# Performance work log

Hardware: AMD Instinct MI355X
Metric: run time of the kernel (lower is better)

Reference implementation:

```python
import jax, jax.numpy as jnp
import numpy as np

H, D = 16, 64  # num_heads, head_dim (hidden=1024)


def _rel_shift(x):
    # Transformer-XL skewing: x [B,H,T,L] -> shifted [B,H,T,T]
    B, Hh, T, L = x.shape
    x = jnp.pad(x, ((0, 0), (0, 0), (0, 0), (1, 0)))
    x = x.reshape(B, Hh, L + 1, T)[:, :, 1:, :]
    return x.reshape(B, Hh, T, L)[:, :, :, :T]


def setup_inputs() -> dict:
    key = jax.random.key(0)
    ks = jax.random.split(key, 9)
    B, T, hid = 2, 2048, 1024
    s = 0.02
    return {
        "x": jax.random.normal(ks[0], (B, T, hid), jnp.float32),
        "pos_emb": jax.random.normal(ks[1], (T, hid), jnp.float32),
        "Wq": jax.random.normal(ks[2], (hid, hid), jnp.float32) * s,
        "Wk": jax.random.normal(ks[3], (hid, hid), jnp.float32) * s,
        "Wv": jax.random.normal(ks[4], (hid, hid), jnp.float32) * s,
        "Wo": jax.random.normal(ks[5], (hid, hid), jnp.float32) * s,
        "Wrel": jax.random.normal(ks[6], (hid, hid), jnp.float32) * s,
        "bias_u": jax.random.normal(ks[7], (H, D), jnp.float32) * s,
        "bias_v": jax.random.normal(ks[8], (H, D), jnp.float32) * s,
    }


def reference(x, pos_emb, Wq, Wk, Wv, Wo, Wrel, bias_u, bias_v):
    B, T, hid = x.shape
    scale = D ** (-0.5)
    # projections (torch Linear: y = x @ W.T), reshape to [B,H,T,D]
    q = (x @ Wq.T).reshape(B, T, H, D).transpose(0, 2, 1, 3)
    k = (x @ Wk.T).reshape(B, T, H, D).transpose(0, 2, 1, 3)
    v = (x @ Wv.T).reshape(B, T, H, D).transpose(0, 2, 1, 3)
    # content score with bias_u
    content = jnp.einsum('bhtd,bhsd->bhts', q + bias_u[None, :, None, :], k)
    # positional score with bias_v against projected relative keys [H,L,D]
    rel_k = (pos_emb @ Wrel.T).reshape(-1, H, D).transpose(1, 0, 2)
    pos_score = jnp.einsum('bhtd,hld->bhtl', q + bias_v[None, :, None, :], rel_k)
    pos_score = _rel_shift(pos_score)
    scores = (content + pos_score) * scale
    attn = jax.nn.softmax(scores, axis=-1)
    out = jnp.einsum('bhts,bhsd->bhtd', attn, v)
    out = out.transpose(0, 2, 1, 3).reshape(B, T, hid)
    return out @ Wo.T
```

## Files before the change

kernel.cpp:

```cpp
#include <hip/hip_runtime.h>
#include <hip/hip_bf16.h>

#define T_SEQ 2048
#define HID   1024
#define NH    16
#define HD    64
#define NB    2

typedef __bf16 bf16_t;
typedef bf16_t bf16x8 __attribute__((ext_vector_type(8)));
typedef bf16_t bf16x4 __attribute__((ext_vector_type(4)));
typedef float  f32x4  __attribute__((ext_vector_type(4)));

static __device__ __forceinline__ f32x4 mfma16(bf16x8 a, bf16x8 b, f32x4 c) {
    return __builtin_amdgcn_mfma_f32_16x16x32_bf16(a, b, c, 0, 0, 0);
}

static __device__ __forceinline__ void gll16(const bf16_t* g, bf16_t* l) {
    __builtin_amdgcn_global_load_lds(
        (const __attribute__((address_space(1))) void*)g,
        (__attribute__((address_space(3))) void*)l, 16, 0, 0);
}

__global__ __launch_bounds__(256) void cvt_all(
    const float* __restrict__ x, const float* __restrict__ pos,
    const float* __restrict__ wq, const float* __restrict__ wk,
    const float* __restrict__ wv, const float* __restrict__ wo,
    const float* __restrict__ wrel,
    bf16_t* __restrict__ xb, bf16_t* __restrict__ pb,
    bf16_t* __restrict__ wqb, bf16_t* __restrict__ wkb,
    bf16_t* __restrict__ wvb, bf16_t* __restrict__ wob,
    bf16_t* __restrict__ wrelb)
{
    int blk = blockIdx.x;
    const float* in; bf16_t* out;
    if (blk < 2048)      { in = x;   out = xb; }
    else if (blk < 3072) { in = pos; out = pb; blk -= 2048; }
    else {
        const int wi = (blk - 3072) >> 9; blk = (blk - 3072) & 511;
        switch (wi) {
            case 0:  in = wq;   out = wqb;   break;
            case 1:  in = wk;   out = wkb;   break;
            case 2:  in = wv;   out = wvb;   break;
            case 3:  in = wo;   out = wob;   break;
            default: in = wrel; out = wrelb; break;
        }
    }
    const int i = blk * 256 + threadIdx.x;
    const float4* p = (const float4*)(in + (size_t)i * 8);
    float4 a0 = p[0], a1 = p[1];
    bf16x8 v;
    v[0]=(bf16_t)a0.x; v[1]=(bf16_t)a0.y; v[2]=(bf16_t)a0.z; v[3]=(bf16_t)a0.w;
    v[4]=(bf16_t)a1.x; v[5]=(bf16_t)a1.y; v[6]=(bf16_t)a1.z; v[7]=(bf16_t)a1.w;
    *(bf16x8*)(out + (size_t)i * 8) = v;
}

template<int OMODE>
__global__ __launch_bounds__(256) void gemm_bb(const bf16_t* __restrict__ A,
                                               const bf16_t* __restrict__ W,
                                               void* __restrict__ outv, int M, int cpx) {
    const int hw = blockIdx.x;
    const int logical = (hw & 7) * cpx + (hw >> 3);
    const int mt = logical >> 3, nt = logical & 7;
    const int row0 = mt * 128, col0 = nt * 128;
    const int tid = threadIdx.x;
    const int w = tid >> 6, lane = tid & 63;
    const int wr = (w >> 1) * 64, wc = (w & 1) * 64;
    const int lr = lane & 15, lkg = lane >> 4;
    const int kd = lkg * 8;

    __shared__ bf16_t Al[128*64];
    __shared__ bf16_t Bl[128*64];

    const int rsh   = lane >> 3;
    const int colSw = ((lane & 7) * 8) ^ (rsh << 3);
    const int rBase = 8*w + rsh;

    f32x4 acc[4][4] = {};

    for (int t = 0; t < 16; ++t) {
        const int k0 = t * 64;
        if (t) __syncthreads();
#pragma unroll
        for (int i = 0; i < 4; ++i) {
            const int r = rBase + 32*i;
            gll16(A + (size_t)(row0 + r)*HID + k0 + colSw, &Al[i*2048 + w*512]);
            gll16(W + (size_t)(col0 + r)*HID + k0 + colSw, &Bl[i*2048 + w*512]);
        }
        __syncthreads();
#pragma unroll
        for (int ks = 0; ks < 2; ++ks) {
            bf16x8 af[4], bq[4];
#pragma unroll
            for (int i = 0; i < 4; ++i) {
                const int ar = wr + i*16 + lr;
                af[i] = *(const bf16x8*)&Al[ar*64 + ((ks*32 + kd) ^ ((ar & 7) << 3))];
                const int br = wc + i*16 + lr;
                bq[i] = *(const bf16x8*)&Bl[br*64 + ((ks*32 + kd) ^ ((br & 7) << 3))];
            }
#pragma unroll
            for (int i = 0; i < 4; ++i)
#pragma unroll
                for (int j = 0; j < 4; ++j)
                    acc[i][j] = mfma16(af[i], bq[j], acc[i][j]);
        }
    }

    const int rb = lkg * 4;
#pragma unroll
    for (int i = 0; i < 4; ++i) {
#pragma unroll
        for (int j = 0; j < 4; ++j) {
            const int col = col0 + wc + j*16 + lr;
            const int row = row0 + wr + i*16 + rb;
            if (OMODE == 0) {
                bf16_t* ob = (bf16_t*)outv;
#pragma unroll
                for (int r = 0; r < 4; ++r)
                    ob[(size_t)(row + r) * HID + col] = (bf16_t)acc[i][j][r];
            } else if (OMODE == 1) {
                const int bb = row >> 11, tt = row & (T_SEQ - 1);
                const int hh = col >> 6,  d = col & 63;
                bf16x4 pk;
#pragma unroll
                for (int r = 0; r < 4; ++r) pk[r] = (bf16_t)acc[i][j][r];
                *(bf16x4*)((bf16_t*)outv + ((size_t)((bb*NH + hh)*HD + d))*T_SEQ + tt) = pk;
            } else {
                float* of = (float*)outv;
#pragma unroll
                for (int r = 0; r < 4; ++r)
                    of[(size_t)(row + r) * HID + col] = acc[i][j][r];
            }
        }
    }
}

template<int NSPLIT>
__global__ __launch_bounds__(256) void attn_kernel(
    const bf16_t* __restrict__ Q, const bf16_t* __restrict__ K,
    const bf16_t* __restrict__ VT, const bf16_t* __restrict__ RK,
    const float* __restrict__ bias_u, const float* __restrict__ bias_v,
    bf16_t* __restrict__ AO, float* __restrict__ PO, float* __restrict__ ML,
    int cpx)
{
    const int hw = blockIdx.x;
    const int logical = (hw & 7) * cpx + (hw >> 3);
    const int tile = logical & 31;
    int h, b, split;
    if (NSPLIT == 1) {
        split = 0; h = (logical >> 5) & 15; b = logical >> 9;
    } else {
        split = (logical >> 5) & 1; h = (logical >> 6) & 15; b = logical >> 10;
    }

    const int w = threadIdx.x >> 6, lane = threadIdx.x & 63;
    const int t0 = tile * 64;
    const int lr = lane & 15, lkg = lane >> 4;
    const int kd = lkg * 8;

    __shared__ bf16_t Kl[64*64];
    __shared__ bf16_t Vl[64*64];
    __shared__ bf16_t R1l[128*64];
    __shared__ bf16_t R2l[128*64];
    __shared__ float  pp[4][16][84];
    __shared__ bf16_t pl[4][16][72];

    const int tb = t0 + w * 16;

    bf16x8 aqu[2], aqv[2], aqv2[2];
    {
        const int t  = tb + lr;
        const int t2 = (t + 1 < T_SEQ) ? t + 1 : T_SEQ - 1;
        const bf16_t* qp  = Q + ((size_t)(b*T_SEQ + t )*NH + h)*HD;
        const bf16_t* qp2 = Q + ((size_t)(b*T_SEQ + t2)*NH + h)*HD;
        const float* bu = bias_u + h*HD;
        const float* bv = bias_v + h*HD;
#pragma unroll
        for (int f = 0; f < 2; ++f) {
            const int k0 = f*32 + kd;
            bf16x8 q1 = *(const bf16x8*)(qp  + k0);
            bf16x8 q2 = *(const bf16x8*)(qp2 + k0);
#pragma unroll
            for (int j = 0; j < 8; ++j) {
                const float fu = bu[k0+j], fv = bv[k0+j];
                aqu [f][j] = (bf16_t)(((float)q1[j] + fu) * 0.125f);
                aqv [f][j] = (bf16_t)(((float)q1[j] + fv) * 0.125f);
                aqv2[f][j] = (bf16_t)(((float)q2[j] + fv) * 0.125f);
            }
        }
    }

    float m_run = -1e30f, l_run = 0.0f;
    f32x4 oacc[4];
    f32x4 zf = {0.f, 0.f, 0.f, 0.f};
#pragma unroll
    for (int nf = 0; nf < 4; ++nf) oacc[nf] = zf;

    const bf16_t* Kb = K  + (size_t)(b*T_SEQ)*HID + h*HD;
    const bf16_t* Vb = VT + (size_t)((b*NH + h)*HD)*T_SEQ;
    const bf16_t* Rb = RK + h*HD;
    const int d15 = 15 - lr;
    const int sBeg = split * (T_SEQ / NSPLIT);

    const int rsh   = lane >> 3;
    const int colSw = ((lane & 7) * 8) ^ (rsh << 3);
    const int kvRow = 16*w + rsh;
    const int rRow  = 32*w + rsh;

    for (int ss = 0; ss < T_SEQ / NSPLIT; ss += 64) {
        const int s0 = sBeg + ss;
        const int r1base = s0 - t0 + T_SEQ - 64;
        const int r2base = s0 - t0 - 65;
        const bool anyB1 = (s0 <= t0 + 63);
        const bool anyB2 = (s0 >= t0 - 61);

        __syncthreads();
#pragma unroll
        for (int i = 0; i < 2; ++i) {
            const int r = kvRow + 8*i;
            gll16(Kb + (size_t)(s0 + r)*HID + colSw, &Kl[(2*w + i)*512]);
            gll16(Vb + (size_t)r*T_SEQ + s0 + colSw, &Vl[(2*w + i)*512]);
        }
        if (anyB1) {
#pragma unroll
            for (int i = 0; i < 4; ++i) {
                const long g = (long)(r1base + rRow + 8*i);
                gll16(Rb + g*HID + colSw, &R1l[(4*w + i)*512]);
            }
        }
        if (anyB2) {
#pragma unroll
            for (int i = 0; i < 4; ++i) {
                const long g = (long)(r2base + rRow + 8*i);
                gll16(Rb + g*HID + colSw, &R2l[(4*w + i)*512]);
            }
        }
        __syncthreads();

        f32x4 sc[4];
#pragma unroll
        for (int j = 0; j < 4; ++j) {
            const int row = j*16 + lr;
            const int sw = (row & 7) << 3;
            bf16x8 a0 = *(const bf16x8*)&Kl[row*64 + (kd ^ sw)];
            bf16x8 a1 = *(const bf16x8*)&Kl[row*64 + ((32 + kd) ^ sw)];
            sc[j] = mfma16(a1, aqu[1], mfma16(a0, aqu[0], zf));
        }

        if (s0 <= tb + 15) {
#pragma unroll
            for (int jf = 0; jf < 5; ++jf) {
                const int rr = 48 - 16*w + jf*16 + lr;
                const int sw = (rr & 7) << 3;
                bf16x8 a0 = *(const bf16x8*)&R1l[rr*64 + (kd ^ sw)];
                bf16x8 a1 = *(const bf16x8*)&R1l[rr*64 + ((32 + kd) ^ sw)];
                f32x4 c = mfma16(a1, aqv[1], mfma16(a0, aqv[0], zf));
                *(f32x4*)&pp[w][lr][jf*16 + 4*lkg] = c;
            }
            if (s0 <= tb - 63) {
#pragma unroll
                for (int j = 0; j < 4; ++j)
#pragma unroll
                    for (int r = 0; r < 4; ++r)
                        sc[j][r] += pp[w][lr][16*j + 4*lkg + r + d15];
            } else {
#pragma unroll
                for (int j = 0; j < 4; ++j)
#pragma unroll
                    for (int r = 0; r < 4; ++r) {
                        const int sof = 16*j + 4*lkg + r;
                        const int dt  = (s0 + sof) - (tb + lr);
                        const float v = pp[w][lr][sof + d15];
                        sc[j][r] += (dt <= 0) ? v : 0.0f;
                    }
            }
        }
        if (s0 >= tb - 61) {
#pragma unroll
            for (int jf = 0; jf < 5; ++jf) {
                const int rr = 48 - 16*w + jf*16 + lr;
                const int sw = (rr & 7) << 3;
                bf16x8 a0 = *(const bf16x8*)&R2l[rr*64 + (kd ^ sw)];
                bf16x8 a1 = *(const bf16x8*)&R2l[rr*64 + ((32 + kd) ^ sw)];
                f32x4 c = mfma16(a1, aqv2[1], mfma16(a0, aqv2[0], zf));
                *(f32x4*)&pp[w][lr][jf*16 + 4*lkg] = c;
            }
            if (s0 >= tb + 17) {
#pragma unroll
                for (int j = 0; j < 4; ++j)
#pragma unroll
                    for (int r = 0; r < 4; ++r)
                        sc[j][r] += pp[w][lr][16*j + 4*lkg + r + d15];
            } else {
#pragma unroll
                for (int j = 0; j < 4; ++j)
#pragma unroll
                    for (int r = 0; r < 4; ++r) {
                        const int sof = 16*j + 4*lkg + r;
                        const int dt  = (s0 + sof) - (tb + lr);
                        const float v = pp[w][lr][sof + d15];
                        sc[j][r] += (dt >= 2) ? v : 0.0f;
                    }
            }
        }

        float mx = fmaxf(fmaxf(fmaxf(sc[0][0], sc[0][1]), fmaxf(sc[0][2], sc[0][3])),
                         fmaxf(fmaxf(sc[1][0], sc[1][1]), fmaxf(sc[1][2], sc[1][3])));
        mx = fmaxf(mx, fmaxf(fmaxf(fmaxf(sc[2][0], sc[2][1]), fmaxf(sc[2][2], sc[2][3])),
                             fmaxf(fmaxf(sc[3][0], sc[3][1]), fmaxf(sc[3][2], sc[3][3]))));
        mx = fmaxf(mx, __shfl_xor(mx, 16, 64));
        mx = fmaxf(mx, __shfl_xor(mx, 32, 64));
        const float mnew = fmaxf(m_run, mx);
        const float fac = __expf(m_run - mnew);
        float sum = 0.0f;
#pragma unroll
        for (int j = 0; j < 4; ++j) {
            bf16x4 pk;
#pragma unroll
            for (int r = 0; r < 4; ++r) {
                const float p = __expf(sc[j][r] - mnew);
                sum += p;
                pk[r] = (bf16_t)p;
            }
            *(bf16x4*)&pl[w][lr][16*j + 4*lkg] = pk;
        }
        sum += __shfl_xor(sum, 16, 64);
        sum += __shfl_xor(sum, 32, 64);
        l_run = l_run * fac + sum;
        m_run = mnew;

#pragma unroll
        for (int r = 0; r < 4; ++r) {
            const float facq = __shfl(fac, 4*lkg + r, 64);
#pragma unroll
            for (int nf = 0; nf < 4; ++nf) oacc[nf][r] *= facq;
        }

        bf16x8 pa0 = *(const bf16x8*)(&pl[w][lr][kd]);
        bf16x8 pa1 = *(const bf16x8*)(&pl[w][lr][32 + kd]);
#pragma unroll
        for (int nf = 0; nf < 4; ++nf) {
            const int row = nf*16 + lr;
            const int sw = (row & 7) << 3;
            bf16x8 b0 = *(const bf16x8*)&Vl[row*64 + (kd ^ sw)];
            bf16x8 b1 = *(const bf16x8*)&Vl[row*64 + ((32 + kd) ^ sw)];
            oacc[nf] = mfma16(pa1, b1, mfma16(pa0, b0, oacc[nf]));
        }
    }

    if (NSPLIT == 1) {
        const float linv = 1.0f / l_run;
#pragma unroll
        for (int r = 0; r < 4; ++r) {
            const float lq = __shfl(linv, 4*lkg + r, 64);
            const int t = tb + 4*lkg + r;
#pragma unroll
            for (int nf = 0; nf < 4; ++nf)
                AO[(size_t)(b*T_SEQ + t)*HID + h*HD + nf*16 + lr] = (bf16_t)(oacc[nf][r] * lq);
        }
    } else {
        float* po = PO + (((size_t)split*NB*NH + b*NH + h)*T_SEQ)*HD;
#pragma unroll
        for (int r = 0; r < 4; ++r)
#pragma unroll
            for (int nf = 0; nf < 4; ++nf)
                po[(size_t)(tb + 4*lkg + r)*HD + nf*16 + lr] = oacc[nf][r];
        if (lkg == 0) {
            float* ml = ML + ((size_t)split*NB*NH + b*NH + h)*2*T_SEQ;
            ml[tb + lr] = m_run;
            ml[T_SEQ + tb + lr] = l_run;
        }
    }
}

__global__ __launch_bounds__(256) void combine_kernel(
    const float* __restrict__ PO, const float* __restrict__ ML,
    bf16_t* __restrict__ AO)
{
    const int idx = blockIdx.x * 256 + threadIdx.x;
    const int t = idx & (T_SEQ - 1);
    const int h = (idx >> 11) & (NH - 1);
    const int b = idx >> 15;
    const size_t poS = (size_t)NB*NH*T_SEQ*HD;
    const size_t mlS = (size_t)NB*NH*2*T_SEQ;
    const float* po1 = PO + (((size_t)b*NH + h)*T_SEQ + t)*HD;
    const float* po2 = po1 + poS;
    const float* ml1 = ML + ((size_t)b*NH + h)*2*T_SEQ;
    const float* ml2 = ml1 + mlS;
    const float m1 = ml1[t], l1 = ml1[T_SEQ + t];
    const float m2 = ml2[t], l2 = ml2[T_SEQ + t];
    const float M  = fmaxf(m1, m2);
    float f1 = __expf(m1 - M), f2 = __expf(m2 - M);
    const float linv = 1.0f / (f1*l1 + f2*l2);
    f1 *= linv; f2 *= linv;
    bf16_t* ao = AO + ((size_t)b*T_SEQ + t)*HID + h*HD;
#pragma unroll
    for (int d = 0; d < HD; d += 8) {
        f32x4 a0 = *(const f32x4*)(po1 + d), a1 = *(const f32x4*)(po1 + d + 4);
        f32x4 c0 = *(const f32x4*)(po2 + d), c1 = *(const f32x4*)(po2 + d + 4);
        bf16x8 o;
#pragma unroll
        for (int j = 0; j < 4; ++j) {
            o[j]     = (bf16_t)(f1*a0[j] + f2*c0[j]);
            o[4 + j] = (bf16_t)(f1*a1[j] + f2*c1[j]);
        }
        *(bf16x8*)(ao + d) = o;
    }
}

extern "C" void kernel_launch(void* const* d_in, const int* in_sizes, int n_in,
                              void* d_out, int out_size, void* d_ws, size_t ws_size,
                              hipStream_t stream) {
    const float* x    = (const float*)d_in[0];
    const float* pos  = (const float*)d_in[1];
    const float* Wq   = (const float*)d_in[2];
    const float* Wk   = (const float*)d_in[3];
    const float* Wv   = (const float*)d_in[4];
    const float* Wo   = (const float*)d_in[5];
    const float* Wrel = (const float*)d_in[6];
    const float* bu   = (const float*)d_in[7];
    const float* bv   = (const float*)d_in[8];

    bf16_t* ws   = (bf16_t*)d_ws;
    const size_t M1 = 1024u * 1024u;
    bf16_t* qb    = ws;
    bf16_t* kb    = ws + 4*M1;
    bf16_t* vtb   = ws + 8*M1;
    bf16_t* rkb   = ws + 12*M1;
    bf16_t* ab    = ws + 14*M1;
    bf16_t* xb    = ab;
    bf16_t* pb    = ws + 18*M1;
    bf16_t* wqb   = ws + 20*M1;
    bf16_t* wkb   = ws + 21*M1;
    bf16_t* wvb   = ws + 22*M1;
    bf16_t* wob   = ws + 23*M1;
    bf16_t* wrelb = ws + 24*M1;

    const size_t baseBytes = 25*M1*2;
    const size_t poBytes = (size_t)2*NB*NH*T_SEQ*HD*4;
    const size_t mlBytes = (size_t)2*NB*NH*2*T_SEQ*4;
    float* PO = (float*)((char*)d_ws + baseBytes);
    float* ML = (float*)((char*)d_ws + baseBytes + poBytes);
    const bool split2 = ws_size >= baseBytes + poBytes + mlBytes;

    cvt_all<<<5632, 256, 0, stream>>>(x, pos, Wq, Wk, Wv, Wo, Wrel,
                                      xb, pb, wqb, wkb, wvb, wob, wrelb);

    gemm_bb<0><<<256, 256, 0, stream>>>(xb, wqb,   qb,  4096, 32);
    gemm_bb<0><<<256, 256, 0, stream>>>(xb, wkb,   kb,  4096, 32);
    gemm_bb<1><<<256, 256, 0, stream>>>(xb, wvb,   vtb, 4096, 32);
    gemm_bb<0><<<128, 256, 0, stream>>>(pb, wrelb, rkb, 2048, 16);

    if (split2) {
        attn_kernel<2><<<2048, 256, 0, stream>>>(qb, kb, vtb, rkb, bu, bv, ab, PO, ML, 256);
        combine_kernel<<<256, 256, 0, stream>>>(PO, ML, ab);
    } else {
        attn_kernel<1><<<1024, 256, 0, stream>>>(qb, kb, vtb, rkb, bu, bv, ab, nullptr, nullptr, 128);
    }

    gemm_bb<2><<<256, 256, 0, stream>>>(ab, wob, d_out, 4096, 32);
}
```

Baseline: 264.8 us.

## Double-buffer GEMM LDS tiles and merge four projection GEMMs into one launch

The GEMM main loop now uses two LDS buffers, so the global-to-LDS loads for the next K tile are issued while MFMAs run on the current tile, with one barrier per iteration. The Q, K, V and relative-key projection GEMMs are combined into a single 896-block launch that picks its operands per block, which removes three launches and their tail idle time. Doubling the LDS footprint to 64KB per block may lower occupancy. The output mode becomes a runtime branch rather than a template parameter.

```diff
diff --git a/kernel.cpp b/kernel.cpp
--- a/kernel.cpp
+++ b/kernel.cpp
@@ -55,48 +55,51 @@
     *(bf16x8*)(out + (size_t)i * 8) = v;
 }
 
-template<int OMODE>
-__global__ __launch_bounds__(256) void gemm_bb(const bf16_t* __restrict__ A,
-                                               const bf16_t* __restrict__ W,
-                                               void* __restrict__ outv, int M, int cpx) {
-    const int hw = blockIdx.x;
-    const int logical = (hw & 7) * cpx + (hw >> 3);
-    const int mt = logical >> 3, nt = logical & 7;
-    const int row0 = mt * 128, col0 = nt * 128;
+static __device__ __forceinline__ void gemm_core(
+    bf16_t* Al, bf16_t* Bl,
+    const bf16_t* __restrict__ A, const bf16_t* __restrict__ W,
+    void* __restrict__ outv, int row0, int col0, int omode)
+{
     const int tid = threadIdx.x;
     const int w = tid >> 6, lane = tid & 63;
     const int wr = (w >> 1) * 64, wc = (w & 1) * 64;
     const int lr = lane & 15, lkg = lane >> 4;
     const int kd = lkg * 8;
-
-    __shared__ bf16_t Al[128*64];
-    __shared__ bf16_t Bl[128*64];
-
     const int rsh   = lane >> 3;
     const int colSw = ((lane & 7) * 8) ^ (rsh << 3);
     const int rBase = 8*w + rsh;
 
     f32x4 acc[4][4] = {};
 
+#pragma unroll
+    for (int i = 0; i < 4; ++i) {
+        const int r = rBase + 32*i;
+        gll16(A + (size_t)(row0 + r)*HID + colSw, &Al[i*2048 + w*512]);
+        gll16(W + (size_t)(col0 + r)*HID + colSw, &Bl[i*2048 + w*512]);
+    }
+    __syncthreads();
+
     for (int t = 0; t < 16; ++t) {
-        const int k0 = t * 64;
-        if (t) __syncthreads();
-#pragma unroll
-        for (int i = 0; i < 4; ++i) {
-            const int r = rBase + 32*i;
-            gll16(A + (size_t)(row0 + r)*HID + k0 + colSw, &Al[i*2048 + w*512]);
-            gll16(W + (size_t)(col0 + r)*HID + k0 + colSw, &Bl[i*2048 + w*512]);
-        }
-        __syncthreads();
+        const int cur = (t & 1) * 8192;
+        const int nxt = 8192 - cur;
+        if (t < 15) {
+            const int k0 = (t + 1) * 64;
+#pragma unroll
+            for (int i = 0; i < 4; ++i) {
+                const int r = rBase + 32*i;
+                gll16(A + (size_t)(row0 + r)*HID + k0 + colSw, &Al[nxt + i*2048 + w*512]);
+                gll16(W + (size_t)(col0 + r)*HID + k0 + colSw, &Bl[nxt + i*2048 + w*512]);
+            }
+        }
 #pragma unroll
         for (int ks = 0; ks < 2; ++ks) {
             bf16x8 af[4], bq[4];
 #pragma unroll
             for (int i = 0; i < 4; ++i) {
                 const int ar = wr + i*16 + lr;
-                af[i] = *(const bf16x8*)&Al[ar*64 + ((ks*32 + kd) ^ ((ar & 7) << 3))];
+                af[i] = *(const bf16x8*)&Al[cur + ar*64 + ((ks*32 + kd) ^ ((ar & 7) << 3))];
                 const int br = wc + i*16 + lr;
-                bq[i] = *(const bf16x8*)&Bl[br*64 + ((ks*32 + kd) ^ ((br & 7) << 3))];
+                bq[i] = *(const bf16x8*)&Bl[cur + br*64 + ((ks*32 + kd) ^ ((br & 7) << 3))];
             }
 #pragma unroll
             for (int i = 0; i < 4; ++i)
@@ -104,6 +107,7 @@
                 for (int j = 0; j < 4; ++j)
                     acc[i][j] = mfma16(af[i], bq[j], acc[i][j]);
         }
+        __syncthreads();
     }
 
     const int rb = lkg * 4;
@@ -113,12 +117,12 @@
         for (int j = 0; j < 4; ++j) {
             const int col = col0 + wc + j*16 + lr;
             const int row = row0 + wr + i*16 + rb;
-            if (OMODE == 0) {
+            if (omode == 0) {
                 bf16_t* ob = (bf16_t*)outv;
 #pragma unroll
                 for (int r = 0; r < 4; ++r)
                     ob[(size_t)(row + r) * HID + col] = (bf16_t)acc[i][j][r];
-            } else if (OMODE == 1) {
+            } else if (omode == 1) {
                 const int bb = row >> 11, tt = row & (T_SEQ - 1);
                 const int hh = col >> 6,  d = col & 63;
                 bf16x4 pk;
@@ -133,6 +137,38 @@
             }
         }
     }
+}
+
+__global__ __launch_bounds__(256) void gemm_proj(
+    const bf16_t* __restrict__ xb, const bf16_t* __restrict__ pb,
+    const bf16_t* __restrict__ wqb, const bf16_t* __restrict__ wkb,
+    const bf16_t* __restrict__ wvb, const bf16_t* __restrict__ wrelb,
+    bf16_t* __restrict__ qb, bf16_t* __restrict__ kb,
+    bf16_t* __restrict__ vtb, bf16_t* __restrict__ rkb)
+{
+    __shared__ bf16_t Al[2*128*64];
+    __shared__ bf16_t Bl[2*128*64];
+    const int hw = blockIdx.x;
+    const int logical = (hw & 7) * 112 + (hw >> 3);
+    const bf16_t* A; const bf16_t* W; void* out; int omode = 0; int l;
+    if (logical < 256)      { A = xb; W = wqb;   out = qb;  l = logical; }
+    else if (logical < 512) { A = xb; W = wkb;   out = kb;  l = logical - 256; }
+    else if (logical < 768) { A = xb; W = wvb;   out = vtb; l = logical - 512; omode = 1; }
+    else                    { A = pb; W = wrelb; out = rkb; l = logical - 768; }
+    const int row0 = (l >> 3) * 128, col0 = (l & 7) * 128;
+    gemm_core(Al, Bl, A, W, out, row0, col0, omode);
+}
+
+__global__ __launch_bounds__(256) void gemm_out(
+    const bf16_t* __restrict__ ab, const bf16_t* __restrict__ wob,
+    float* __restrict__ outp)
+{
+    __shared__ bf16_t Al[2*128*64];
+    __shared__ bf16_t Bl[2*128*64];
+    const int hw = blockIdx.x;
+    const int logical = (hw & 7) * 32 + (hw >> 3);
+    const int row0 = (logical >> 3) * 128, col0 = (logical & 7) * 128;
+    gemm_core(Al, Bl, ab, wob, outp, row0, col0, 2);
 }
 
 template<int NSPLIT>
@@ -446,10 +482,8 @@
     cvt_all<<<5632, 256, 0, stream>>>(x, pos, Wq, Wk, Wv, Wo, Wrel,
                                       xb, pb, wqb, wkb, wvb, wob, wrelb);
 
-    gemm_bb<0><<<256, 256, 0, stream>>>(xb, wqb,   qb,  4096, 32);
-    gemm_bb<0><<<256, 256, 0, stream>>>(xb, wkb,   kb,  4096, 32);
-    gemm_bb<1><<<256, 256, 0, stream>>>(xb, wvb,   vtb, 4096, 32);
-    gemm_bb<0><<<128, 256, 0, stream>>>(pb, wrelb, rkb, 2048, 16);
+    gemm_proj<<<896, 256, 0, stream>>>(xb, pb, wqb, wkb, wvb, wrelb,
+                                       qb, kb, vtb, rkb);
 
     if (split2) {
         attn_kernel<2><<<2048, 256, 0, stream>>>(qb, kb, vtb, rkb, bu, bv, ab, PO, ML, 256);
@@ -458,5 +492,5 @@
         attn_kernel<1><<<1024, 256, 0, stream>>>(qb, kb, vtb, rkb, bu, bv, ab, nullptr, nullptr, 128);
     }
 
-    gemm_bb<2><<<256, 256, 0, stream>>>(ab, wob, d_out, 4096, 32);
-}
+    gemm_out<<<256, 256, 0, stream>>>(ab, wob, (float*)d_out);
+}
```

Result: faster. 248.4 us (-6.2%).
